# Optimization experiments

Hardware: AMD Instinct MI355X
Metric: run time of the kernel (lower is better)

Reference implementation:

```python
import jax, jax.numpy as jnp
import numpy as np
import math

B, S, D, H = 4, 2048, 1024, 16
DH = D // H  # 64
EPS = 1e-5


def setup_inputs() -> dict:
    key = jax.random.key(0)
    ks = jax.random.split(key, 8)
    s = 1.0 / math.sqrt(D)
    return {
        "x": jax.random.normal(ks[0], (B, S, D), dtype=jnp.float32),
        "key_val_lengths": jax.random.randint(ks[1], (B,), 1, S + 1),  # >=1 so no fully-masked row
        "Wq": jax.random.uniform(ks[2], (D, D), jnp.float32, -s, s),
        "bq": jnp.zeros((D,), jnp.float32),
        "Wkv": jax.random.uniform(ks[3], (2 * D, D), jnp.float32, -s, s),
        "bkv": jnp.zeros((2 * D,), jnp.float32),
        "Wo": jax.random.uniform(ks[4], (D, D), jnp.float32, -s, s),
        "bo": jnp.zeros((D,), jnp.float32),
        "ln_g": jnp.ones((D,), jnp.float32),
        "ln_b": jnp.zeros((D,), jnp.float32),
    }


def reference(x, key_val_lengths, Wq, bq, Wkv, bkv, Wo, bo, ln_g, ln_b):
    # Causal self-attention path (query_seq == key_val_seq, is_decoder=True),
    # dropout in eval mode (identity). Faithful to the torch module's math.
    skip = x
    # LayerNorm (applied to both query and key/value since self-attention)
    mu = jnp.mean(x, axis=-1, keepdims=True)
    var = jnp.mean(jnp.square(x - mu), axis=-1, keepdims=True)
    xn = (x - mu) * jax.lax.rsqrt(var + EPS) * ln_g + ln_b

    q = xn @ Wq.T + bq                      # [B,S,D]
    kv = xn @ Wkv.T + bkv                   # [B,S,2D]
    k, v = kv[..., :D], kv[..., D:]

    q = q.reshape(B, S, H, DH)
    k = k.reshape(B, S, H, DH)
    v = v.reshape(B, S, H, DH)

    scores = jnp.einsum("bqhd,bkhd->bhqk", q, k) / math.sqrt(DH)  # [B,H,S,S]

    # padding mask on keys fused with causal mask
    key_pos = jnp.arange(S)
    pad_ok = (key_pos[None, :] < key_val_lengths[:, None])[:, None, None, :]  # [B,1,1,S]
    causal = (key_pos[None, :] <= key_pos[:, None])[None, None, :, :]         # [1,1,S,S]
    scores = jnp.where(pad_ok & causal, scores, -jnp.inf)

    attn = jax.nn.softmax(scores, axis=-1)
    out = jnp.einsum("bhqk,bkhd->bqhd", attn, v).reshape(B, S, D)
    return out @ Wo.T + bo + skip
```

## Files before the change

### kernel.cpp

```cpp
#include <hip/hip_runtime.h>
#include <hip/hip_bf16.h>


#define Bn 4
#define Sn 2048
#define Dn 1024
#define Hn 16
#define DHn 64
#define Mn (Bn*Sn)

typedef short short8 __attribute__((ext_vector_type(8)));
typedef short short4v __attribute__((ext_vector_type(4)));
typedef unsigned short ushort8 __attribute__((ext_vector_type(8)));
typedef unsigned short ushort4v __attribute__((ext_vector_type(4)));
typedef float f32x4 __attribute__((ext_vector_type(4)));

__device__ inline float bf2f(unsigned short u) {
    union { unsigned int i; float f; } c;
    c.i = ((unsigned int)u) << 16;
    return c.f;
}

__device__ inline unsigned short f2bf(float f) {
    union { float f; unsigned int i; } c;
    c.f = f;
    unsigned int i = c.i;
    unsigned int lsb = (i >> 16) & 1;
    i += 0x7fffu + lsb;
    return (unsigned short)(i >> 16);
}

__device__ inline unsigned short f2bf_t(float f) {
    union { float f; unsigned int i; } c;
    c.f = f;
    return (unsigned short)(c.i >> 16);
}

__device__ __forceinline__ float fast_exp2(float x) {
#if __has_builtin(__builtin_amdgcn_exp2f)
    return __builtin_amdgcn_exp2f(x);
#else
    return exp2f(x);
#endif
}

#if __has_builtin(__builtin_amdgcn_global_load_lds)
#define HAVE_GLDS 1
__device__ __forceinline__ void glds16(const void* g, void* l) {
    __builtin_amdgcn_global_load_lds(
        (const __attribute__((address_space(1))) unsigned int*)g,
        (__attribute__((address_space(3))) unsigned int*)l, 16, 0, 0);
}
#else
#define HAVE_GLDS 0
#endif

__global__ __launch_bounds__(256) void f2bf3_kernel(const float* __restrict__ Wq,
                                                    const float* __restrict__ Wkv,
                                                    const float* __restrict__ Wo,
                                                    unsigned short* __restrict__ oq,
                                                    unsigned short* __restrict__ okv,
                                                    unsigned short* __restrict__ oo) {
    int i = blockIdx.x * 256 + threadIdx.x;
    const float* src;
    unsigned short* dst;
    int off;
    if (i < 262144) { src = Wq; dst = oq; off = i; }
    else if (i < 786432) { src = Wkv; dst = okv; off = i - 262144; }
    else { src = Wo; dst = oo; off = i - 786432; }
    float4 v = *(const float4*)(src + (size_t)off * 4);
    ushort4v r;
    r.x = f2bf(v.x); r.y = f2bf(v.y); r.z = f2bf(v.z); r.w = f2bf(v.w);
    *(ushort4v*)(dst + (size_t)off * 4) = r;
}

__global__ __launch_bounds__(256) void ln_kernel(const float* __restrict__ x,
                                                 const float* __restrict__ g,
                                                 const float* __restrict__ bta,
                                                 unsigned short* __restrict__ xn) {
    int row = blockIdx.x;
    int t = threadIdx.x;
    const float* xr = x + (size_t)row * Dn;
    float4 v = *(const float4*)(xr + t * 4);
    float s = v.x + v.y + v.z + v.w;
    float sq = v.x * v.x + v.y * v.y + v.z * v.z + v.w * v.w;
    for (int off = 32; off; off >>= 1) {
        s += __shfl_down(s, off);
        sq += __shfl_down(sq, off);
    }
    __shared__ float ss[4], ssq[4];
    int wave = t >> 6, lane = t & 63;
    if (lane == 0) { ss[wave] = s; ssq[wave] = sq; }
    __syncthreads();
    float tot = ss[0] + ss[1] + ss[2] + ss[3];
    float totq = ssq[0] + ssq[1] + ssq[2] + ssq[3];
    float mean = tot * (1.0f / Dn);
    float var = totq * (1.0f / Dn) - mean * mean;
    float rstd = rsqrtf(var + 1e-5f);
    float4 gv = *(const float4*)(g + t * 4);
    float4 bv = *(const float4*)(bta + t * 4);
    ushort4v r;
    r.x = f2bf((v.x - mean) * rstd * gv.x + bv.x);
    r.y = f2bf((v.y - mean) * rstd * gv.y + bv.y);
    r.z = f2bf((v.z - mean) * rstd * gv.z + bv.z);
    r.w = f2bf((v.w - mean) * rstd * gv.w + bv.w);
    *(ushort4v*)(xn + (size_t)row * Dn + t * 4) = r;
}

template <bool ADD_SKIP, bool OUT_BF16>
__global__ __launch_bounds__(256, 2) void gemm_bt(const unsigned short* __restrict__ A,
                                                  const unsigned short* __restrict__ Bw,
                                                  const float* __restrict__ bias,
                                                  const float* __restrict__ bias2,
                                                  int bsplit,
                                                  const float* __restrict__ skip,
                                                  void* __restrict__ Cout,
                                                  int M, int N, int K) {
    __shared__ unsigned short As[128 * 32];
    __shared__ unsigned short Bs[128 * 32];
    const int tid = threadIdx.x;
    const int wave = tid >> 6, lane = tid & 63;
    const int warp_m = wave & 1, warp_n = wave >> 1;
    const int bm = blockIdx.x, bn = blockIdx.y;
    const int l4 = lane & 3, lr = lane >> 2;
    const int quad = lane >> 4, r16 = lane & 15;

    f32x4 acc[4][4];
#pragma unroll
    for (int i = 0; i < 4; i++)
#pragma unroll
        for (int j = 0; j < 4; j++) acc[i][j] = (f32x4){0.f, 0.f, 0.f, 0.f};

    for (int k0 = 0; k0 < K; k0 += 32) {
        __syncthreads();
#if HAVE_GLDS
#pragma unroll
        for (int i = 0; i < 2; ++i) {
            int inst = wave + 4 * i;
            glds16(A + (size_t)(bm * 128 + inst * 16 + lr) * K + k0 + l4 * 8, &As[inst * 512]);
            glds16(Bw + (size_t)(bn * 128 + inst * 16 + lr) * K + k0 + l4 * 8, &Bs[inst * 512]);
        }
#else
#pragma unroll
        for (int i = 0; i < 2; ++i) {
            int inst = wave + 4 * i;
            int row = inst * 16 + lr;
            ushort8 a = *(const ushort8*)(A + (size_t)(bm * 128 + row) * K + k0 + l4 * 8);
            ushort8 b2 = *(const ushort8*)(Bw + (size_t)(bn * 128 + row) * K + k0 + l4 * 8);
            *(ushort8*)(As + inst * 512 + lane * 8) = a;
            *(ushort8*)(Bs + inst * 512 + lane * 8) = b2;
        }
#endif
        __syncthreads();

        short8 afr[4], bfr[4];
#pragma unroll
        for (int i = 0; i < 4; ++i) {
            int row = warp_m * 64 + i * 16 + r16;
            afr[i] = *(const short8*)(As + row * 32 + quad * 8);
        }
#pragma unroll
        for (int j = 0; j < 4; ++j) {
            int row = warp_n * 64 + j * 16 + r16;
            bfr[j] = *(const short8*)(Bs + row * 32 + quad * 8);
        }
#pragma unroll
        for (int i = 0; i < 4; ++i)
#pragma unroll
            for (int j = 0; j < 4; ++j)
                acc[i][j] = __builtin_amdgcn_mfma_f32_16x16x32_bf16(afr[i], bfr[j], acc[i][j], 0, 0, 0);
    }

    const float* bp = (bn * 128 >= bsplit) ? (bias2 - bsplit) : bias;
#pragma unroll
    for (int j = 0; j < 4; ++j) {
        int gcol = bn * 128 + warp_n * 64 + j * 16 + r16;
        float bv = bp[gcol];
#pragma unroll
        for (int i = 0; i < 4; ++i) {
#pragma unroll
            for (int r = 0; r < 4; ++r) {
                int grow = bm * 128 + warp_m * 64 + i * 16 + quad * 4 + r;
                float v = acc[i][j][r] + bv;
                size_t idx = (size_t)grow * N + gcol;
                if (ADD_SKIP) v += skip[idx];
                if (OUT_BF16)
                    ((unsigned short*)Cout)[idx] = f2bf(v);
                else
                    ((float*)Cout)[idx] = v;
            }
        }
    }
}

#define STK 72
#define STV 68
#define STP 72
#define QKVS (3 * Dn)

__global__ __launch_bounds__(256, 4) void attn_kernel(const unsigned short* __restrict__ QKV,
                                                      const int* __restrict__ lens,
                                                      unsigned short* __restrict__ Ctx) {
    const int h = blockIdx.y, b = blockIdx.z;
    const int qtA = blockIdx.x;
    const int qtB = (Sn / 64 - 1) - qtA;
    const int tid = threadIdx.x;
    const int wave = tid >> 6, lane = tid & 63;
    const int quad = lane >> 4, c = lane & 15;
    const int len = lens[b];
    const int lt = (len - 1) >> 6;
    const int ktendA = min(qtA, lt);
    const int ktendB = min(qtB, lt);
    const int qwA = qtA * 64 + wave * 16;
    const int qwB = qtB * 64 + wave * 16;
    const int myqA = qwA + c, myqB = qwB + c;

    __shared__ unsigned short Ks[64 * STK];
    __shared__ unsigned short Vt[64 * STV];
    __shared__ unsigned short Ps[4][16 * STP];

    short8 qfA[2], qfB[2];
    {
        const unsigned short* qa = QKV + (size_t)(b * Sn + qwA + c) * QKVS + h * 64 + quad * 8;
        qfA[0] = *(const short8*)(qa);
        qfA[1] = *(const short8*)(qa + 32);
        const unsigned short* qb = QKV + (size_t)(b * Sn + qwB + c) * QKVS + h * 64 + quad * 8;
        qfB[0] = *(const short8*)(qb);
        qfB[1] = *(const short8*)(qb + 32);
    }

    f32x4 accA[4], accB[4];
#pragma unroll
    for (int j = 0; j < 4; j++) {
        accA[j] = (f32x4){0.f, 0.f, 0.f, 0.f};
        accB[j] = (f32x4){0.f, 0.f, 0.f, 0.f};
    }
    float mA = -1e30f, lA = 0.f, mB = -1e30f, lB = 0.f;

    const int krow = tid >> 2, dp = tid & 3;
    const int kg = tid >> 4, dg = tid & 15;
    const unsigned short* kbase = QKV + (size_t)(b * Sn) * QKVS + Dn + h * 64;
    const unsigned short* vbase = QKV + (size_t)(b * Sn) * QKVS + 2 * Dn + h * 64;

    ushort8 kr0, kr1;
    ushort4v vr0, vr1, vr2, vr3;
    {
        const unsigned short* kp2 = kbase + (size_t)krow * QKVS + dp * 16;
        kr0 = *(const ushort8*)(kp2);
        kr1 = *(const ushort8*)(kp2 + 8);
        const unsigned short* vp2 = vbase + (size_t)(kg * 4) * QKVS + dg * 4;
        vr0 = *(const ushort4v*)(vp2);
        vr1 = *(const ushort4v*)(vp2 + QKVS);
        vr2 = *(const ushort4v*)(vp2 + 2 * QKVS);
        vr3 = *(const ushort4v*)(vp2 + 3 * QKVS);
    }

    const float C2 = 0.18033688011112042f;

    auto process = [&](int kt, const short8* qf, f32x4* acc_o, float& m_run, float& l_run,
                       int qw, int myq) {
        f32x4 sacc[4];
#pragma unroll
        for (int mt = 0; mt < 4; ++mt) sacc[mt] = (f32x4){0.f, 0.f, 0.f, 0.f};
#pragma unroll
        for (int mt = 0; mt < 4; ++mt) {
            short8 kf0 = *(const short8*)(&Ks[(mt * 16 + c) * STK + quad * 8]);
            short8 kf1 = *(const short8*)(&Ks[(mt * 16 + c) * STK + 32 + quad * 8]);
            sacc[mt] = __builtin_amdgcn_mfma_f32_16x16x32_bf16(kf0, qf[0], sacc[mt], 0, 0, 0);
            sacc[mt] = __builtin_amdgcn_mfma_f32_16x16x32_bf16(kf1, qf[1], sacc[mt], 0, 0, 0);
        }

        const int kb = kt * 64;
        const bool full = (kb + 63 <= qw) && (kb + 64 <= len);
        float sv[16];
        float mx = -1e30f;
        if (full) {
#pragma unroll
            for (int e = 0; e < 16; ++e) {
                float v = sacc[e >> 2][e & 3];
                sv[e] = v;
                mx = fmaxf(mx, v);
            }
        } else {
#pragma unroll
            for (int mt = 0; mt < 4; ++mt) {
#pragma unroll
                for (int r = 0; r < 4; ++r) {
                    int kpos = kb + mt * 16 + quad * 4 + r;
                    bool valid = (kpos <= myq) && (kpos < len);
                    float v = valid ? sacc[mt][r] : -1e30f;
                    sv[mt * 4 + r] = v;
                    mx = fmaxf(mx, v);
                }
            }
        }
        mx = fmaxf(mx, __shfl_xor(mx, 16));
        mx = fmaxf(mx, __shfl_xor(mx, 32));
        float mnew = fmaxf(m_run, mx * C2);
        float alpha = fast_exp2(m_run - mnew);
        m_run = mnew;
        l_run *= alpha;

        float ar_[4];
#pragma unroll
        for (int r = 0; r < 4; ++r) ar_[r] = __shfl(alpha, quad * 4 + r);
#pragma unroll
        for (int j = 0; j < 4; ++j)
#pragma unroll
            for (int r = 0; r < 4; ++r) acc_o[j][r] *= ar_[r];

#pragma unroll
        for (int mt = 0; mt < 4; ++mt) {
            float p0 = fast_exp2(__builtin_fmaf(sv[mt * 4 + 0], C2, -mnew));
            float p1 = fast_exp2(__builtin_fmaf(sv[mt * 4 + 1], C2, -mnew));
            float p2 = fast_exp2(__builtin_fmaf(sv[mt * 4 + 2], C2, -mnew));
            float p3 = fast_exp2(__builtin_fmaf(sv[mt * 4 + 3], C2, -mnew));
            l_run += (p0 + p1) + (p2 + p3);
            ushort4v pw;
            pw.x = f2bf_t(p0); pw.y = f2bf_t(p1); pw.z = f2bf_t(p2); pw.w = f2bf_t(p3);
            *(ushort4v*)(&Ps[wave][c * STP + mt * 16 + quad * 4]) = pw;
        }

#pragma unroll
        for (int ks = 0; ks < 2; ++ks) {
            short8 pf = *(const short8*)(&Ps[wave][c * STP + ks * 32 + quad * 8]);
#pragma unroll
            for (int j = 0; j < 4; ++j) {
                const unsigned short* vb2 = &Vt[(j * 16 + c) * STV + ks * 32 + quad * 8];
                short4v a0 = *(const short4v*)(vb2);
                short4v a1 = *(const short4v*)(vb2 + 4);
                short8 vf = __builtin_shufflevector(a0, a1, 0, 1, 2, 3, 4, 5, 6, 7);
                acc_o[j] = __builtin_amdgcn_mfma_f32_16x16x32_bf16(pf, vf, acc_o[j], 0, 0, 0);
            }
        }
    };

    for (int kt = 0; kt <= ktendB; ++kt) {
        __syncthreads();
        *(ushort8*)(&Ks[krow * STK + dp * 16]) = kr0;
        *(ushort8*)(&Ks[krow * STK + dp * 16 + 8]) = kr1;
#pragma unroll
        for (int w = 0; w < 4; ++w) {
            ushort4v t;
            t.x = vr0[w]; t.y = vr1[w]; t.z = vr2[w]; t.w = vr3[w];
            *(ushort4v*)(&Vt[(dg * 4 + w) * STV + kg * 4]) = t;
        }
        __syncthreads();

        if (kt < ktendB) {
            const unsigned short* kp2 = kbase + (size_t)((kt + 1) * 64 + krow) * QKVS + dp * 16;
            kr0 = *(const ushort8*)(kp2);
            kr1 = *(const ushort8*)(kp2 + 8);
            const unsigned short* vp2 = vbase + (size_t)((kt + 1) * 64 + kg * 4) * QKVS + dg * 4;
            vr0 = *(const ushort4v*)(vp2);
            vr1 = *(const ushort4v*)(vp2 + QKVS);
            vr2 = *(const ushort4v*)(vp2 + 2 * QKVS);
            vr3 = *(const ushort4v*)(vp2 + 3 * QKVS);
        }

        if (kt <= ktendA)
            process(kt, qfA, accA, mA, lA, qwA, myqA);
        process(kt, qfB, accB, mB, lB, qwB, myqB);
    }

    auto finalize = [&](f32x4* acc_o, float l_run, int qw) {
        l_run += __shfl_xor(l_run, 16);
        l_run += __shfl_xor(l_run, 32);
        float li[4];
#pragma unroll
        for (int r = 0; r < 4; ++r) {
            float lv = __shfl(l_run, quad * 4 + r);
            li[r] = 1.0f / lv;
        }
#pragma unroll
        for (int r = 0; r < 4; ++r) {
            unsigned short* cp = Ctx + ((size_t)(b * Sn + qw + quad * 4 + r)) * Dn + h * 64 + c;
#pragma unroll
            for (int j = 0; j < 4; ++j) {
                cp[j * 16] = f2bf(acc_o[j][r] * li[r]);
            }
        }
    };
    finalize(accA, lA, qwA);
    finalize(accB, lB, qwB);
}

extern "C" void kernel_launch(void* const* d_in, const int* in_sizes, int n_in,
                              void* d_out, int out_size, void* d_ws, size_t ws_size,
                              hipStream_t stream) {
    const float* x = (const float*)d_in[0];
    const int* lens = (const int*)d_in[1];
    const float* Wq = (const float*)d_in[2];
    const float* bq = (const float*)d_in[3];
    const float* Wkv = (const float*)d_in[4];
    const float* bkv = (const float*)d_in[5];
    const float* Wo = (const float*)d_in[6];
    const float* bo = (const float*)d_in[7];
    const float* ln_g = (const float*)d_in[8];
    const float* ln_b = (const float*)d_in[9];
    float* out = (float*)d_out;

    char* ws = (char*)d_ws;
    unsigned short* xn_bf = (unsigned short*)ws;
    unsigned short* wq_bf = (unsigned short*)(ws + (size_t)16 * 1024 * 1024);
    unsigned short* wkv_bf = (unsigned short*)(ws + (size_t)18 * 1024 * 1024);
    unsigned short* wo_bf = (unsigned short*)(ws + (size_t)22 * 1024 * 1024);
    unsigned short* qkv_bf = (unsigned short*)(ws + (size_t)24 * 1024 * 1024);
    unsigned short* ctx_bf = (unsigned short*)(ws + (size_t)72 * 1024 * 1024);

    f2bf3_kernel<<<4096, 256, 0, stream>>>(Wq, Wkv, Wo, wq_bf, wkv_bf, wo_bf);

    ln_kernel<<<Mn, 256, 0, stream>>>(x, ln_g, ln_b, xn_bf);

    {
        dim3 grid(Mn / 128, 3 * Dn / 128);
        gemm_bt<false, true><<<grid, 256, 0, stream>>>(xn_bf, wq_bf, bq, bkv, Dn, nullptr,
                                                       (void*)qkv_bf, Mn, 3 * Dn, Dn);
    }
    {
        dim3 grid(Sn / 128, Hn, Bn);
        attn_kernel<<<grid, 256, 0, stream>>>(qkv_bf, lens, ctx_bf);
    }
    {
        dim3 grid(Mn / 128, Dn / 128);
        gemm_bt<true, false><<<grid, 256, 0, stream>>>(ctx_bf, wo_bf, bo, bo, Dn, x,
                                                       (void*)out, Mn, Dn, Dn);
    }
}
```

Before: 270.2 us.

## Fuse weight cast into LayerNorm kernel, deepen GEMM K-step, remap attention grid

Merges the weight fp32-to-bf16 conversion and the LayerNorm into one launch, removing one kernel launch and its tail. The GEMM now stages 64 K-elements per barrier pair (two 32-wide LDS slabs), halving the number of sync points at the cost of doubled LDS per block. The attention grid is flattened so batch and head vary fastest, which interleaves blocks with different sequence lengths across CUs for better load balance and L2 locality.

After: 277.4 us. +2.7%, slower.

```diff
diff --git a/kernel.cpp b/kernel.cpp
--- a/kernel.cpp
+++ b/kernel.cpp
@@ -55,31 +55,32 @@
 #define HAVE_GLDS 0
 #endif
 
-__global__ __launch_bounds__(256) void f2bf3_kernel(const float* __restrict__ Wq,
-                                                    const float* __restrict__ Wkv,
-                                                    const float* __restrict__ Wo,
-                                                    unsigned short* __restrict__ oq,
-                                                    unsigned short* __restrict__ okv,
-                                                    unsigned short* __restrict__ oo) {
-    int i = blockIdx.x * 256 + threadIdx.x;
-    const float* src;
-    unsigned short* dst;
-    int off;
-    if (i < 262144) { src = Wq; dst = oq; off = i; }
-    else if (i < 786432) { src = Wkv; dst = okv; off = i - 262144; }
-    else { src = Wo; dst = oo; off = i - 786432; }
-    float4 v = *(const float4*)(src + (size_t)off * 4);
-    ushort4v r;
-    r.x = f2bf(v.x); r.y = f2bf(v.y); r.z = f2bf(v.z); r.w = f2bf(v.w);
-    *(ushort4v*)(dst + (size_t)off * 4) = r;
-}
-
-__global__ __launch_bounds__(256) void ln_kernel(const float* __restrict__ x,
-                                                 const float* __restrict__ g,
-                                                 const float* __restrict__ bta,
-                                                 unsigned short* __restrict__ xn) {
-    int row = blockIdx.x;
-    int t = threadIdx.x;
+__global__ __launch_bounds__(256) void prep_kernel(const float* __restrict__ x,
+                                                   const float* __restrict__ g,
+                                                   const float* __restrict__ bta,
+                                                   unsigned short* __restrict__ xn,
+                                                   const float* __restrict__ Wq,
+                                                   const float* __restrict__ Wkv,
+                                                   const float* __restrict__ Wo,
+                                                   unsigned short* __restrict__ oq,
+                                                   unsigned short* __restrict__ okv,
+                                                   unsigned short* __restrict__ oo) {
+    const int t = threadIdx.x;
+    if (blockIdx.x >= Mn) {
+        int i = (blockIdx.x - Mn) * 256 + t;
+        const float* src;
+        unsigned short* dst;
+        int off;
+        if (i < 262144) { src = Wq; dst = oq; off = i; }
+        else if (i < 786432) { src = Wkv; dst = okv; off = i - 262144; }
+        else { src = Wo; dst = oo; off = i - 786432; }
+        float4 v = *(const float4*)(src + (size_t)off * 4);
+        ushort4v r;
+        r.x = f2bf(v.x); r.y = f2bf(v.y); r.z = f2bf(v.z); r.w = f2bf(v.w);
+        *(ushort4v*)(dst + (size_t)off * 4) = r;
+        return;
+    }
+    const int row = blockIdx.x;
     const float* xr = x + (size_t)row * Dn;
     float4 v = *(const float4*)(xr + t * 4);
     float s = v.x + v.y + v.z + v.w;
@@ -116,8 +117,8 @@
                                                   const float* __restrict__ skip,
                                                   void* __restrict__ Cout,
                                                   int M, int N, int K) {
-    __shared__ unsigned short As[128 * 32];
-    __shared__ unsigned short Bs[128 * 32];
+    __shared__ unsigned short As[2 * 128 * 32];
+    __shared__ unsigned short Bs[2 * 128 * 32];
     const int tid = threadIdx.x;
     const int wave = tid >> 6, lane = tid & 63;
     const int warp_m = wave & 1, warp_n = wave >> 1;
@@ -131,44 +132,55 @@
 #pragma unroll
         for (int j = 0; j < 4; j++) acc[i][j] = (f32x4){0.f, 0.f, 0.f, 0.f};
 
-    for (int k0 = 0; k0 < K; k0 += 32) {
+    for (int k0 = 0; k0 < K; k0 += 64) {
         __syncthreads();
 #if HAVE_GLDS
 #pragma unroll
-        for (int i = 0; i < 2; ++i) {
-            int inst = wave + 4 * i;
-            glds16(A + (size_t)(bm * 128 + inst * 16 + lr) * K + k0 + l4 * 8, &As[inst * 512]);
-            glds16(Bw + (size_t)(bn * 128 + inst * 16 + lr) * K + k0 + l4 * 8, &Bs[inst * 512]);
+        for (int ks = 0; ks < 2; ++ks) {
+#pragma unroll
+            for (int i = 0; i < 2; ++i) {
+                int inst = wave + 4 * i;
+                glds16(A + (size_t)(bm * 128 + inst * 16 + lr) * K + k0 + ks * 32 + l4 * 8,
+                       &As[ks * 4096 + inst * 512]);
+                glds16(Bw + (size_t)(bn * 128 + inst * 16 + lr) * K + k0 + ks * 32 + l4 * 8,
+                       &Bs[ks * 4096 + inst * 512]);
+            }
         }
 #else
 #pragma unroll
-        for (int i = 0; i < 2; ++i) {
-            int inst = wave + 4 * i;
-            int row = inst * 16 + lr;
-            ushort8 a = *(const ushort8*)(A + (size_t)(bm * 128 + row) * K + k0 + l4 * 8);
-            ushort8 b2 = *(const ushort8*)(Bw + (size_t)(bn * 128 + row) * K + k0 + l4 * 8);
-            *(ushort8*)(As + inst * 512 + lane * 8) = a;
-            *(ushort8*)(Bs + inst * 512 + lane * 8) = b2;
+        for (int ks = 0; ks < 2; ++ks) {
+#pragma unroll
+            for (int i = 0; i < 2; ++i) {
+                int inst = wave + 4 * i;
+                int row = inst * 16 + lr;
+                ushort8 a = *(const ushort8*)(A + (size_t)(bm * 128 + row) * K + k0 + ks * 32 + l4 * 8);
+                ushort8 b2 = *(const ushort8*)(Bw + (size_t)(bn * 128 + row) * K + k0 + ks * 32 + l4 * 8);
+                *(ushort8*)(As + ks * 4096 + inst * 512 + lane * 8) = a;
+                *(ushort8*)(Bs + ks * 4096 + inst * 512 + lane * 8) = b2;
+            }
         }
 #endif
         __syncthreads();
 
-        short8 afr[4], bfr[4];
-#pragma unroll
-        for (int i = 0; i < 4; ++i) {
-            int row = warp_m * 64 + i * 16 + r16;
-            afr[i] = *(const short8*)(As + row * 32 + quad * 8);
-        }
-#pragma unroll
-        for (int j = 0; j < 4; ++j) {
-            int row = warp_n * 64 + j * 16 + r16;
-            bfr[j] = *(const short8*)(Bs + row * 32 + quad * 8);
-        }
-#pragma unroll
-        for (int i = 0; i < 4; ++i)
-#pragma unroll
-            for (int j = 0; j < 4; ++j)
-                acc[i][j] = __builtin_amdgcn_mfma_f32_16x16x32_bf16(afr[i], bfr[j], acc[i][j], 0, 0, 0);
+#pragma unroll
+        for (int ks = 0; ks < 2; ++ks) {
+            short8 afr[4], bfr[4];
+#pragma unroll
+            for (int i = 0; i < 4; ++i) {
+                int row = warp_m * 64 + i * 16 + r16;
+                afr[i] = *(const short8*)(As + ks * 4096 + row * 32 + quad * 8);
+            }
+#pragma unroll
+            for (int j = 0; j < 4; ++j) {
+                int row = warp_n * 64 + j * 16 + r16;
+                bfr[j] = *(const short8*)(Bs + ks * 4096 + row * 32 + quad * 8);
+            }
+#pragma unroll
+            for (int i = 0; i < 4; ++i)
+#pragma unroll
+                for (int j = 0; j < 4; ++j)
+                    acc[i][j] = __builtin_amdgcn_mfma_f32_16x16x32_bf16(afr[i], bfr[j], acc[i][j], 0, 0, 0);
+        }
     }
 
     const float* bp = (bn * 128 >= bsplit) ? (bias2 - bsplit) : bias;
@@ -201,8 +213,9 @@
 __global__ __launch_bounds__(256, 4) void attn_kernel(const unsigned short* __restrict__ QKV,
                                                       const int* __restrict__ lens,
                                                       unsigned short* __restrict__ Ctx) {
-    const int h = blockIdx.y, b = blockIdx.z;
-    const int qtA = blockIdx.x;
+    const int b = blockIdx.x & 3;
+    const int h = (blockIdx.x >> 2) & 15;
+    const int qtA = blockIdx.x >> 6;
     const int qtB = (Sn / 64 - 1) - qtA;
     const int tid = threadIdx.x;
     const int wave = tid >> 6, lane = tid & 63;
@@ -408,9 +421,8 @@
     unsigned short* qkv_bf = (unsigned short*)(ws + (size_t)24 * 1024 * 1024);
     unsigned short* ctx_bf = (unsigned short*)(ws + (size_t)72 * 1024 * 1024);
 
-    f2bf3_kernel<<<4096, 256, 0, stream>>>(Wq, Wkv, Wo, wq_bf, wkv_bf, wo_bf);
-
-    ln_kernel<<<Mn, 256, 0, stream>>>(x, ln_g, ln_b, xn_bf);
+    prep_kernel<<<Mn + 4096, 256, 0, stream>>>(x, ln_g, ln_b, xn_bf,
+                                               Wq, Wkv, Wo, wq_bf, wkv_bf, wo_bf);
 
     {
         dim3 grid(Mn / 128, 3 * Dn / 128);
@@ -418,8 +430,7 @@
                                                        (void*)qkv_bf, Mn, 3 * Dn, Dn);
     }
     {
-        dim3 grid(Sn / 128, Hn, Bn);
-        attn_kernel<<<grid, 256, 0, stream>>>(qkv_bf, lens, ctx_bf);
+        attn_kernel<<<(Sn / 128) * Hn * Bn, 256, 0, stream>>>(qkv_bf, lens, ctx_bf);
     }
     {
         dim3 grid(Mn / 128, Dn / 128);
```
